# Kernel tuning notes

Hardware: AMD Instinct MI355X
Metric: run time of the kernel (lower is better)

## Reference

```python
import jax, jax.numpy as jnp
import numpy as np

EOS = 1  # EOS_VALUE in the original code (word_label == 1 triggers end_sentence)
L_LAYERS = 2
B, T, H, E = 128, 256, 1024, 1024  # TD == E == input_size


def setup_inputs() -> dict:
    key = jax.random.key(0)
    ks = jax.random.split(key, 20)
    k = 1.0 / np.sqrt(H)
    u = lambda kk, shape: jax.random.uniform(kk, shape, jnp.float32, -k, k)
    inp = {
        "yy_pad": jax.random.randint(ks[0], (B, T), 0, E, dtype=jnp.int32),
        "h_t": jax.random.normal(ks[1], (L_LAYERS, B, H), jnp.float32),
        "h_t_rev": jax.random.normal(ks[2], (L_LAYERS, B, H), jnp.float32),
        "x_lens": jax.random.randint(ks[3], (B,), 1, T - 1, dtype=jnp.int32).at[0].set(T - 1),
        # parameters (layer 0 input size == E == H, so weights stack cleanly)
        "emb": jax.random.normal(ks[4], (E, E), jnp.float32) * 0.02,
        "W_ih": u(ks[5], (L_LAYERS, 4 * H, E)),
        "W_hh": u(ks[6], (L_LAYERS, 4 * H, H)),
        "b_ih": u(ks[7], (L_LAYERS, 4 * H)),
        "b_hh": u(ks[8], (L_LAYERS, 4 * H)),
        "W_ih_rev": u(ks[9], (L_LAYERS, 4 * H, E)),
        "W_hh_rev": u(ks[10], (L_LAYERS, 4 * H, H)),
        "b_ih_rev": u(ks[11], (L_LAYERS, 4 * H)),
        "b_hh_rev": u(ks[12], (L_LAYERS, 4 * H)),
        "c0": jnp.zeros((L_LAYERS, H), jnp.float32),
        "c0_rev": jnp.zeros((L_LAYERS, H), jnp.float32),
        "fc_W": u(ks[13], (E, 2 * H)),
        "fc_b": u(ks[14], (E,)),
    }
    return inp


def _lstm_cell(x, h, c, Wih, Whh, bih, bhh):
    # torch.nn.LSTMCell gate order: input, forget, cell(g), output
    z = x @ Wih.T + bih + h @ Whh.T + bhh  # [B, 4H]
    i, f, g, o = jnp.split(z, 4, axis=-1)
    c2 = jax.nn.sigmoid(f) * c + jax.nn.sigmoid(i) * jnp.tanh(g)
    h2 = jax.nn.sigmoid(o) * jnp.tanh(c2)
    return h2, c2


def reference(yy_pad, h_t, h_t_rev, x_lens, emb, W_ih, W_hh, b_ih, b_hh,
              W_ih_rev, W_hh_rev, b_ih_rev, b_hh_rev, c0, c0_rev, fc_W, fc_b):
    batch = yy_pad.shape[0]
    n_steps = yy_pad.shape[1]  # == max(x_lens) + 1 by construction (static)
    eos_onehot = jax.nn.one_hot(EOS, fc_W.shape[0], dtype=fc_W.dtype)  # [TD]

    c_init = jnp.broadcast_to(c0[:, None, :], (L_LAYERS, batch, c0.shape[1]))
    c_init_rev = jnp.broadcast_to(c0_rev[:, None, :], (L_LAYERS, batch, c0.shape[1]))

    def step(carry, _):
        feed, h, hr, c, cr, ended = carry
        x = emb[feed]   # [B, E]  (sos embedding / previous argmax token)
        xr = x
        hs, hrs, cs, crs = [], [], [], []
        for l in range(L_LAYERS):
            hn, cn = _lstm_cell(x, h[l], c[l], W_ih[l], W_hh[l], b_ih[l], b_hh[l])
            hrn, crn = _lstm_cell(xr, hr[l], cr[l], W_ih_rev[l], W_hh_rev[l], b_ih_rev[l], b_hh_rev[l])
            hs.append(hn); cs.append(cn); hrs.append(hrn); crs.append(crn)
            x, xr = hn, hrn
        h, hr = jnp.stack(hs), jnp.stack(hrs)
        c, cr = jnp.stack(cs), jnp.stack(crs)
        # faithful to torch: cat([B,H],[B,H]) -> [B,2H] -> permute(1,0) -> reshape(B,-1)
        wh = jnp.concatenate([h[-1], hr[-1]], axis=-1).T.reshape(batch, -1)
        logits = wh @ fc_W.T + fc_b  # [B, TD]
        logits = jnp.where(ended[:, None], eos_onehot, logits)
        label = jnp.argmax(logits, axis=1).astype(jnp.int32)
        ended = ended | (label == EOS)
        return (label, h, hr, c, cr, ended), logits

    carry0 = (yy_pad[:, 0], h_t, h_t_rev, c_init, c_init_rev,
              jnp.zeros((batch,), jnp.bool_))
    _, logits_seq = jax.lax.scan(step, carry0, None, length=n_steps)  # [T, B, TD]
    return jax.nn.softmax(jnp.transpose(logits_seq, (1, 0, 2)), axis=-1)  # [B, T, TD]
```

## Files before the change

### kernel.cpp

```cpp
#include <hip/hip_runtime.h>
#include <math.h>

#define NB 128
#define NT 256
#define NH 1024
#define NE 1024
#define G4 4096
#define EOSL 1

#define C_OFF    ((size_t)0)
#define HT_OFF   ((size_t)524288)
#define FCZ_OFF  ((size_t)786432)
#define BIAS_OFF ((size_t)1835008)
#define END_OFF  ((size_t)1851392)
#define XPH_OFF  ((size_t)1851520)
#define XPX_OFF  ((size_t)2900096)
#define WP_OFF   ((size_t)3031168)
#define TOTAL_MIN_F  ((size_t)3031168)
#define TOTAL_PACK_F ((size_t)36585600)

typedef __attribute__((ext_vector_type(8))) short s8v;
typedef __attribute__((ext_vector_type(4))) float f4v;
typedef __attribute__((ext_vector_type(2))) unsigned u2v;

__device__ __forceinline__ float sigmoid_stable(float x) {
  if (x >= 0.f) return 1.f / (1.f + expf(-x));
  float ex = expf(x);
  return ex / (1.f + ex);
}
__device__ __forceinline__ void add4(float4& d, const float4 a) {
  d.x += a.x; d.y += a.y; d.z += a.z; d.w += a.w;
}
__device__ __forceinline__ unsigned short bf_rne(float x) {
  unsigned u = __float_as_uint(x);
  return (unsigned short)((u + 0x7FFFu + ((u >> 16) & 1u)) >> 16);
}
__device__ __forceinline__ void split_bf(float x, unsigned short& h, unsigned short& l) {
  unsigned u = __float_as_uint(x);
  unsigned hb = (u + 0x7FFFu + ((u >> 16) & 1u)) >> 16;
  h = (unsigned short)hb;
  float r = x - __uint_as_float(hb << 16);
  l = bf_rne(r);
}
__device__ __forceinline__ void cvt8(float4 a0, float4 a1, s8v& hi, s8v& lo)
{
  const float v[8] = {a0.x, a0.y, a0.z, a0.w, a1.x, a1.y, a1.z, a1.w};
  #pragma unroll
  for (int j = 0; j < 8; j++) {
    unsigned short h, l; split_bf(v[j], h, l);
    hi[j] = (short)h; lo[j] = (short)l;
  }
}


__global__ void k_init(const int* yy, const float* h_t, const float* h_tr,
                       const float* c0, const float* c0r,
                       const float* b_ih, const float* b_hh,
                       const float* b_ihr, const float* b_hhr,
                       const float* emb,
                       unsigned short* xph, unsigned short* xpx,
                       float* call, float* bias, int* ended)
{
  int idx = blockIdx.x * 256 + threadIdx.x;
  if (idx < 2 * 2048 * 128) {
    int dir = idx / (2048 * 128); int rem = idx % (2048 * 128);
    int row = rem >> 7, b = rem & 127;
    int l = row >> 10, n = row & 1023;
    const float* src = dir ? h_tr : h_t;
    float v = src[((size_t)l * 128 + b) * 1024 + n];
    unsigned short h, lo; split_bf(v, h, lo);
    size_t off = ((size_t)(dir * 64 + (row >> 5)) * 8 + (b >> 4)) * 1024
               + ((b & 15) + 16 * ((n >> 3) & 3)) * 8 + (n & 7);
    xph[off] = h; xph[off + 512] = lo;
  }
  if (idx < 4 * 1024 * 128) {
    int ld = idx / (1024 * 128); int l = ld >> 1;
    int rem = idx % (1024 * 128);
    int mb = rem >> 10, nl = rem & 7;
    const float* cs = (ld & 1) ? c0r : c0;
    call[idx] = cs[l * 1024 + mb * 8 + nl];
  }
  if (idx < 4 * 4096) {
    int ld = idx / 4096; int l = ld >> 1, dir = ld & 1;
    int m = idx & 4095;
    bias[idx] = (dir ? b_ihr : b_ih)[l * 4096 + m] + (dir ? b_hhr : b_hh)[l * 4096 + m];
  }
  if (idx < 128 * 1024) {
    int b = idx >> 10, k = idx & 1023;
    int e = yy[b * NT];
    float v = emb[(size_t)e * 1024 + k];
    unsigned short h, lo; split_bf(v, h, lo);
    size_t off = ((size_t)(k >> 5) * 8 + (b >> 4)) * 1024
               + ((b & 15) + 16 * ((k >> 3) & 3)) * 8 + (k & 7);
    xpx[off] = h; xpx[off + 512] = lo;
  }
  if (idx < NB) ended[idx] = 0;
}

__global__ void k_packW(const float* W_ih, const float* W_hh,
                        const float* W_ihr, const float* W_hhr,
                        unsigned short* WP)
{
  int idx = blockIdx.x * 256 + threadIdx.x;
  int l = idx & 63;
  int frag = idx >> 6;
  int ktile = frag & 63;
  int mtile = (frag >> 6) & 255;
  int ld = frag >> 14;
  int layer = ld >> 1, dir = ld & 1;
  int s = l & 15;
  int mbb = mtile >> 1, half = mtile & 1;
  int gate = half * 2 + (s >> 3);
  int m = gate * 1024 + mbb * 8 + (s & 7);
  int kg = ktile * 32 + (l >> 4) * 8;
  const float* base;
  if (kg < 1024) base = (dir ? W_ihr : W_ih) + ((size_t)layer * 4096 + m) * 1024 + kg;
  else           base = (dir ? W_hhr : W_hh) + ((size_t)layer * 4096 + m) * 1024 + (kg - 1024);
  float4 a0 = *(const float4*)base, a1 = *(const float4*)(base + 4);
  s8v hi, lo; cvt8(a0, a1, hi, lo);
  unsigned short* outp = WP + (size_t)frag * 1024 + l * 8;
  *(s8v*)outp = hi;
  *(s8v*)(outp + 512) = lo;
}

__device__ __forceinline__ void red_write(float* red, int slot, int l, const f4v (&acc)[2][8])
{
  #pragma unroll
  for (int mt = 0; mt < 2; mt++)
    #pragma unroll
    for (int bt = 0; bt < 8; bt++)
      *(f4v*)&red[(size_t)slot * 4096 + (mt * 8 + bt) * 256 + l * 4] = acc[mt][bt];
}
__device__ __forceinline__ void red_add(const float* red, int slot, int l, f4v (&acc)[2][8])
{
  #pragma unroll
  for (int mt = 0; mt < 2; mt++)
    #pragma unroll
    for (int bt = 0; bt < 8; bt++)
      acc[mt][bt] += *(const f4v*)&red[(size_t)slot * 4096 + (mt * 8 + bt) * 256 + l * 4];
}
__device__ __forceinline__ void gloadW(const unsigned short* Wb, int kk,
                                       s8v (&h)[2], s8v (&lo)[2])
{
  #pragma unroll
  for (int mt = 0; mt < 2; mt++) {
    const unsigned short* q = Wb + ((size_t)(mt * 64 + kk) << 10);
    h[mt] = *(const s8v*)q; lo[mt] = *(const s8v*)(q + 512);
  }
}
__device__ __forceinline__ void gloadB(const unsigned short* Bb, int kk,
                                       s8v (&h)[8], s8v (&lo)[8])
{
  #pragma unroll
  for (int bt = 0; bt < 8; bt++) {
    const unsigned short* q = Bb + ((size_t)(kk * 8 + bt) << 10);
    h[bt] = *(const s8v*)q; lo[bt] = *(const s8v*)(q + 512);
  }
}

template<int PACKED>
__device__ __forceinline__ void gemm_k256(f4v (&acc)[2][8],
                                          const unsigned short* Wb,
                                          const float* Wrow0, const float* Wrow1,
                                          const unsigned short* Bb)
{
  if (PACKED) {
    s8v whc[2], wlc[2];
    gloadW(Wb, 0, whc, wlc);
    #pragma unroll 1
    for (int kk = 0; kk < 8; kk++) {
      s8v bh[8], bl[8];
      gloadB(Bb, kk, bh, bl);
      s8v whn[2], wln[2];
      if (kk < 7) gloadW(Wb, kk + 1, whn, wln);
      #pragma unroll
      for (int mt = 0; mt < 2; mt++)
        #pragma unroll
        for (int bt = 0; bt < 8; bt++) {
          acc[mt][bt] = __builtin_amdgcn_mfma_f32_16x16x32_bf16(whc[mt], bh[bt], acc[mt][bt], 0, 0, 0);
          acc[mt][bt] = __builtin_amdgcn_mfma_f32_16x16x32_bf16(whc[mt], bl[bt], acc[mt][bt], 0, 0, 0);
          acc[mt][bt] = __builtin_amdgcn_mfma_f32_16x16x32_bf16(wlc[mt], bh[bt], acc[mt][bt], 0, 0, 0);
        }
      if (kk < 7) {
        whc[0] = whn[0]; whc[1] = whn[1];
        wlc[0] = wln[0]; wlc[1] = wln[1];
      }
    }
  } else {
    const float* Wrow[2] = { Wrow0, Wrow1 };
    float4 ac[2][2];
    #pragma unroll
    for (int mt = 0; mt < 2; mt++) {
      ac[mt][0] = *(const float4*)(Wrow[mt]);
      ac[mt][1] = *(const float4*)(Wrow[mt] + 4);
    }
    #pragma unroll 1
    for (int kk = 0; kk < 8; kk++) {
      s8v bh[8], bl[8];
      gloadB(Bb, kk, bh, bl);
      float4 an[2][2];
      if (kk < 7) {
        #pragma unroll
        for (int mt = 0; mt < 2; mt++) {
          an[mt][0] = *(const float4*)(Wrow[mt] + (kk + 1) * 32);
          an[mt][1] = *(const float4*)(Wrow[mt] + (kk + 1) * 32 + 4);
        }
      }
      #pragma unroll
      for (int mt = 0; mt < 2; mt++) {
        s8v wh, wl;
        cvt8(ac[mt][0], ac[mt][1], wh, wl);
        #pragma unroll
        for (int bt = 0; bt < 8; bt++) {
          acc[mt][bt] = __builtin_amdgcn_mfma_f32_16x16x32_bf16(wh, bh[bt], acc[mt][bt], 0, 0, 0);
          acc[mt][bt] = __builtin_amdgcn_mfma_f32_16x16x32_bf16(wh, bl[bt], acc[mt][bt], 0, 0, 0);
          acc[mt][bt] = __builtin_amdgcn_mfma_f32_16x16x32_bf16(wl, bh[bt], acc[mt][bt], 0, 0, 0);
        }
      }
      if (kk < 7) {
        #pragma unroll
        for (int mt = 0; mt < 2; mt++) { ac[mt][0] = an[mt][0]; ac[mt][1] = an[mt][1]; }
      }
    }
  }
}

__device__ __forceinline__ void reduce_to_zs(float* lds, int tid, int l, int w,
                                             f4v (&acc)[2][8])
{
  if (w >= 4) red_write(lds, w - 4, l, acc);
  __syncthreads();
  if (w < 4) red_add(lds, w, l, acc);
  __syncthreads();
  if (w == 2 || w == 3) red_write(lds, w - 2, l, acc);
  __syncthreads();
  if (w < 2) red_add(lds, w, l, acc);
  __syncthreads();
  if (w < 2) red_write(lds, w, l, acc);
  __syncthreads();
  float* zs = lds + 8192;
  #pragma unroll
  for (int vi = 0; vi < 2; vi++) {
    int v = tid + vi * 512;
    f4v s = *(const f4v*)&lds[(size_t)v * 4];
    s += *(const f4v*)&lds[4096 + (size_t)v * 4];
    int frag = v >> 6, lane = v & 63;
    int mt = frag >> 3, bt = frag & 7;
    int s0 = (lane >> 4) * 4, bcol = bt * 16 + (lane & 15);
    #pragma unroll
    for (int r = 0; r < 4; r++)
      zs[mt * 2048 + (s0 + r) * 128 + bcol] = s[r];
  }
  __syncthreads();
}

struct CellP {
  const unsigned short* WP;
  const float* Wih; const float* Whh; const float* Wihr; const float* Whhr;
  const float* bias; float* c; const unsigned short* xpx; float* Ht;
};

template<int LAYER, int PACKED>
__global__ __launch_bounds__(512, 2) void k_cell(CellP p, const unsigned short* xpR,
                                                 unsigned short* xpW)
{
  __shared__ __align__(16) float lds[16384];
  const int mb = blockIdx.x, dir = blockIdx.y, tid = threadIdx.x;
  const int l = tid & 63, w = tid >> 6;
  const int lr = l & 15, lk = l >> 4;

  const unsigned short* Bb;
  if (LAYER == 0)
    Bb = (w < 4) ? p.xpx + (size_t)w * 65536
                 : xpR + (size_t)(dir * 64 + (w - 4) * 8) * 8192;
  else
    Bb = (w < 4) ? xpW + (size_t)(dir * 64 + w * 8) * 8192
                 : xpR + (size_t)(dir * 64 + 32 + (w - 4) * 8) * 8192;
  Bb += l * 8;

  f4v acc[2][8];
  #pragma unroll
  for (int mt = 0; mt < 2; mt++)
    #pragma unroll
    for (int bt = 0; bt < 8; bt++)
      acc[mt][bt] = (f4v)(0.0f);

  if (PACKED) {
    const unsigned short* Wb = p.WP + (size_t)(LAYER * 2 + dir) * 16777216ULL
        + (((size_t)(mb * 2) * 64 + (size_t)w * 8) << 10) + l * 8;
    gemm_k256<1>(acc, Wb, nullptr, nullptr, Bb);
  } else {
    const float* Wsel = ((w < 4) ? (dir ? p.Wihr : p.Wih) : (dir ? p.Whhr : p.Whh))
                      + (size_t)LAYER * 4194304;
    int col0 = (w & 3) * 256 + lk * 8;
    const float* Wr0 = Wsel + ((size_t)(((lr >> 3)) * 1024 + mb * 8 + (lr & 7))) * 1024 + col0;
    const float* Wr1 = Wsel + ((size_t)((2 + (lr >> 3)) * 1024 + mb * 8 + (lr & 7))) * 1024 + col0;
    gemm_k256<0>(acc, nullptr, Wr0, Wr1, Bb);
  }

  reduce_to_zs(lds, tid, l, w, acc);
  float* zs = lds + 8192;

  int ldg = LAYER * 2 + dir;
  if (tid < 256) {
    int b = tid & 127, q = tid >> 7;
    float* cp = p.c + ((((size_t)ldg * 128 + mb) * 128 + b) * 8 + q * 4);
    f4v cold = *(const f4v*)cp;
    f4v cnew;
    float hs[4];
    #pragma unroll
    for (int j = 0; j < 4; j++) {
      int nl = q * 4 + j;
      int n = mb * 8 + nl;
      float iv = zs[nl * 128 + b]              + p.bias[ldg * 4096 + n];
      float fv = zs[(nl + 8) * 128 + b]        + p.bias[ldg * 4096 + 1024 + n];
      float gv = zs[2048 + nl * 128 + b]       + p.bias[ldg * 4096 + 2048 + n];
      float ov = zs[2048 + (nl + 8) * 128 + b] + p.bias[ldg * 4096 + 3072 + n];
      float co = cold[j];
      float cn = sigmoid_stable(fv) * co + sigmoid_stable(iv) * tanhf(gv);
      float hn = sigmoid_stable(ov) * tanhf(cn);
      cnew[j] = cn;
      hs[j] = hn;
    }
    *(f4v*)cp = cnew;
    unsigned short hh[4], ll[4];
    #pragma unroll
    for (int j = 0; j < 4; j++) split_bf(hs[j], hh[j], ll[j]);
    int kt = LAYER * 32 + (mb >> 2);
    size_t off = ((size_t)(dir * 64 + kt) * 8 + (b >> 4)) * 1024
               + ((size_t)((b & 15) + 16 * (mb & 3))) * 8 + q * 4;
    u2v vh; vh.x = (unsigned)hh[0] | ((unsigned)hh[1] << 16);
            vh.y = (unsigned)hh[2] | ((unsigned)hh[3] << 16);
    u2v vl; vl.x = (unsigned)ll[0] | ((unsigned)ll[1] << 16);
            vl.y = (unsigned)ll[2] | ((unsigned)ll[3] << 16);
    *(u2v*)(xpW + off) = vh;
    *(u2v*)(xpW + off + 512) = vl;
    if (LAYER == 1) {
      #pragma unroll
      for (int j = 0; j < 4; j++) {
        int n = mb * 8 + q * 4 + j;
        p.Ht[(size_t)dir * 131072 + (size_t)n * 128 + b] = hs[j];
      }
    }
  }
}

__global__ __launch_bounds__(256) void k_fc(const float* Ht, const float* fc_W, float* fcz)
{
  int et = blockIdx.x, kp = blockIdx.y;
  int e0 = et * 64;
  int k00 = kp * 256;
  __shared__ __align__(16) float in_s[128][36];
  __shared__ __align__(16) float w_s[64][36];
  int t = threadIdx.x, e_sub = t & 7, bg = t >> 3, b0 = bg * 4;
  float acc[8][4] = {};
  for (int kc = 0; kc < 256; kc += 32) {
    #pragma unroll
    for (int i = 0; i < 4; i++) {
      int flat = t + 256 * i, r = flat >> 3, f4i = flat & 7;
      const float* row = Ht + (r >= 64 ? (size_t)NH * NB + (size_t)(r - 64) * 2048
                                       : (size_t)r * 2048);
      float4 v = *(const float4*)(row + k00 + kc + f4i * 4);
      int sw = (f4i ^ (r >> 2)) & 7;
      *(float4*)&in_s[r][sw * 4] = v;
    }
    #pragma unroll
    for (int i = 0; i < 2; i++) {
      int flat = t + 256 * i, r = flat >> 3, f4i = flat & 7;
      *(float4*)&w_s[r][f4i * 4] =
          *(const float4*)(fc_W + (size_t)(e0 + r) * 2048 + k00 + kc + f4i * 4);
    }
    __syncthreads();
    #pragma unroll
    for (int kq = 0; kq < 8; kq++) {
      int ksw = (kq ^ bg) & 7;
      float4 a4[4];
      #pragma unroll
      for (int ib = 0; ib < 4; ib++) a4[ib] = *(const float4*)&in_s[b0 + ib][ksw * 4];
      float4 w4[8];
      #pragma unroll
      for (int je = 0; je < 8; je++) w4[je] = *(const float4*)&w_s[e_sub + 8 * je][kq * 4];
      #pragma unroll
      for (int je = 0; je < 8; je++)
        #pragma unroll
        for (int ib = 0; ib < 4; ib++)
          acc[je][ib] += a4[ib].x * w4[je].x + a4[ib].y * w4[je].y +
                         a4[ib].z * w4[je].z + a4[ib].w * w4[je].w;
    }
    __syncthreads();
  }
  for (int je = 0; je < 8; je++) {
    int e = e0 + e_sub + 8 * je;
    for (int ib = 0; ib < 4; ib++)
      fcz[((size_t)kp * NB + b0 + ib) * NE + e] = acc[je][ib];
  }
}

__global__ void k_final(const float* fcz, const float* fc_b, int* ended,
                        float* out, int tstep, const float* emb, unsigned short* xpx)
{
  int b = blockIdx.x;
  int t = threadIdx.x;
  __shared__ float sval[256];
  __shared__ int   sidx[256];
  __shared__ float ssum[256];
  bool end = (ended[b] != 0);
  float v[4];
  int e_base = t * 4;
  float4 vv = *(const float4*)&fc_b[e_base];
  #pragma unroll
  for (int p = 0; p < 8; p++)
    add4(vv, *(const float4*)&fcz[((size_t)p * NB + b) * NE + e_base]);
  v[0] = vv.x; v[1] = vv.y; v[2] = vv.z; v[3] = vv.w;
  if (end) {
    #pragma unroll
    for (int j = 0; j < 4; j++) v[j] = (e_base + j == EOSL) ? 1.f : 0.f;
  }
  float bv = v[0]; int bi = e_base;
  #pragma unroll
  for (int j = 1; j < 4; j++) if (v[j] > bv) { bv = v[j]; bi = e_base + j; }
  sval[t] = bv; sidx[t] = bi;
  __syncthreads();
  for (int s = 128; s > 0; s >>= 1) {
    if (t < s) {
      float ov = sval[t + s]; int oi = sidx[t + s];
      if (ov > sval[t] || (ov == sval[t] && oi < sidx[t])) { sval[t] = ov; sidx[t] = oi; }
    }
    __syncthreads();
  }
  float m = sval[0]; int label = sidx[0];
  {
    int k0 = t * 4;
    float4 e4 = *(const float4*)(emb + (size_t)label * 1024 + k0);
    size_t off = ((size_t)(k0 >> 5) * 8 + (b >> 4)) * 1024
               + ((b & 15) + 16 * ((k0 >> 3) & 3)) * 8 + (k0 & 7);
    ushort4 h4, l4;
    unsigned short hh, ll;
    split_bf(e4.x, hh, ll); h4.x = hh; l4.x = ll;
    split_bf(e4.y, hh, ll); h4.y = hh; l4.y = ll;
    split_bf(e4.z, hh, ll); h4.z = hh; l4.z = ll;
    split_bf(e4.w, hh, ll); h4.w = hh; l4.w = ll;
    *(ushort4*)(xpx + off) = h4;
    *(ushort4*)(xpx + off + 512) = l4;
  }
  float ls = 0.f;
  #pragma unroll
  for (int j = 0; j < 4; j++) { v[j] = expf(v[j] - m); ls += v[j]; }
  ssum[t] = ls;
  __syncthreads();
  for (int s = 128; s > 0; s >>= 1) { if (t < s) ssum[t] += ssum[t + s]; __syncthreads(); }
  float inv = 1.f / ssum[0];
  float* orow = out + ((size_t)b * NT + tstep) * NE + e_base;
  #pragma unroll
  for (int j = 0; j < 4; j++) orow[j] = v[j] * inv;
  if (t == 0) ended[b] = (end || label == EOSL) ? 1 : 0;
}

extern "C" void kernel_launch(void* const* d_in, const int* in_sizes, int n_in,
                              void* d_out, int out_size, void* d_ws, size_t ws_size,
                              hipStream_t stream)
{
  const int*   yy    = (const int*)d_in[0];
  const float* h_t   = (const float*)d_in[1];
  const float* h_tr  = (const float*)d_in[2];
  const float* emb   = (const float*)d_in[4];
  const float* W_ih  = (const float*)d_in[5];
  const float* W_hh  = (const float*)d_in[6];
  const float* b_ih  = (const float*)d_in[7];
  const float* b_hh  = (const float*)d_in[8];
  const float* W_ihr = (const float*)d_in[9];
  const float* W_hhr = (const float*)d_in[10];
  const float* b_ihr = (const float*)d_in[11];
  const float* b_hhr = (const float*)d_in[12];
  const float* c0    = (const float*)d_in[13];
  const float* c0r   = (const float*)d_in[14];
  const float* fc_W  = (const float*)d_in[15];
  const float* fc_b  = (const float*)d_in[16];
  float* out = (float*)d_out;

  float* ws = (float*)d_ws;
  float* call = ws + C_OFF;
  float* Ht   = ws + HT_OFF;
  float* fcz  = ws + FCZ_OFF;
  float* bias = ws + BIAS_OFF;
  int* ended  = (int*)(ws + END_OFF);
  unsigned short* xph = (unsigned short*)(ws + XPH_OFF);
  unsigned short* xpx = (unsigned short*)(ws + XPX_OFF);
  unsigned short* WP  = (unsigned short*)(ws + WP_OFF);
  bool packed = ws_size >= TOTAL_PACK_F * sizeof(float);

  k_init<<<2048, 256, 0, stream>>>(yy, h_t, h_tr, c0, c0r, b_ih, b_hh, b_ihr, b_hhr,
                                   emb, xph, xpx, call, bias, ended);
  if (packed)
    k_packW<<<16384, 256, 0, stream>>>(W_ih, W_hh, W_ihr, W_hhr, WP);

  CellP cp;
  cp.WP = WP;
  cp.Wih = W_ih; cp.Whh = W_hh; cp.Wihr = W_ihr; cp.Whhr = W_hhr;
  cp.bias = bias; cp.c = call; cp.xpx = xpx; cp.Ht = Ht;

  for (int t = 0; t < NT; t++) {
    const unsigned short* xpR = xph + (size_t)(t & 1) * 1048576;
    unsigned short* xpW = xph + (size_t)((t & 1) ^ 1) * 1048576;
    if (packed) {
      k_cell<0, 1><<<dim3(128, 2), 512, 0, stream>>>(cp, xpR, xpW);
      k_cell<1, 1><<<dim3(128, 2), 512, 0, stream>>>(cp, xpR, xpW);
    } else {
      k_cell<0, 0><<<dim3(128, 2), 512, 0, stream>>>(cp, xpR, xpW);
      k_cell<1, 0><<<dim3(128, 2), 512, 0, stream>>>(cp, xpR, xpW);
    }
    k_fc<<<dim3(16, 8), 256, 0, stream>>>(Ht, fc_W, fcz);
    k_final<<<128, 256, 0, stream>>>(fcz, fc_b, ended, out, t, emb, xpx);
  }
}
```

Before: 22.78 ms.

## Halve per-block hidden tile in LSTM cell and double FC split-K

Each cell block now computes 4 hidden units (16 gate rows as one MFMA tile) instead of 8, so the grid doubles to 256x2 blocks. Weight packing, c-state layout and the epilogue are reorganised to match. LDS drops and launch bounds rise to allow more resident blocks. The FC projection is also split into 16 K-chunks instead of 8 for more blocks. The aim is to fill more compute units on this latency-bound recurrent step, at the cost of more partial-sum traffic and narrower scalar stores.

```diff
diff --git a/kernel.cpp b/kernel.cpp
--- a/kernel.cpp
+++ b/kernel.cpp
@@ -11,17 +11,16 @@
 #define C_OFF    ((size_t)0)
 #define HT_OFF   ((size_t)524288)
 #define FCZ_OFF  ((size_t)786432)
-#define BIAS_OFF ((size_t)1835008)
-#define END_OFF  ((size_t)1851392)
-#define XPH_OFF  ((size_t)1851520)
-#define XPX_OFF  ((size_t)2900096)
-#define WP_OFF   ((size_t)3031168)
-#define TOTAL_MIN_F  ((size_t)3031168)
-#define TOTAL_PACK_F ((size_t)36585600)
+#define BIAS_OFF ((size_t)2883584)
+#define END_OFF  ((size_t)2899968)
+#define XPH_OFF  ((size_t)2900096)
+#define XPX_OFF  ((size_t)3948672)
+#define WP_OFF   ((size_t)4079744)
+#define TOTAL_MIN_F  ((size_t)4079744)
+#define TOTAL_PACK_F ((size_t)37634176)
 
 typedef __attribute__((ext_vector_type(8))) short s8v;
 typedef __attribute__((ext_vector_type(4))) float f4v;
-typedef __attribute__((ext_vector_type(2))) unsigned u2v;
 
 __device__ __forceinline__ float sigmoid_stable(float x) {
   if (x >= 0.f) return 1.f / (1.f + expf(-x));
@@ -76,9 +75,9 @@
   if (idx < 4 * 1024 * 128) {
     int ld = idx / (1024 * 128); int l = ld >> 1;
     int rem = idx % (1024 * 128);
-    int mb = rem >> 10, nl = rem & 7;
+    int n = rem >> 7;
     const float* cs = (ld & 1) ? c0r : c0;
-    call[idx] = cs[l * 1024 + mb * 8 + nl];
+    call[idx] = cs[l * 1024 + n];
   }
   if (idx < 4 * 4096) {
     int ld = idx / 4096; int l = ld >> 1, dir = ld & 1;
@@ -105,13 +104,12 @@
   int l = idx & 63;
   int frag = idx >> 6;
   int ktile = frag & 63;
-  int mtile = (frag >> 6) & 255;
+  int mq = (frag >> 6) & 255;
   int ld = frag >> 14;
   int layer = ld >> 1, dir = ld & 1;
   int s = l & 15;
-  int mbb = mtile >> 1, half = mtile & 1;
-  int gate = half * 2 + (s >> 3);
-  int m = gate * 1024 + mbb * 8 + (s & 7);
+  int gate = s >> 2;
+  int m = gate * 1024 + mq * 4 + (s & 3);
   int kg = ktile * 32 + (l >> 4) * 8;
   const float* base;
   if (kg < 1024) base = (dir ? W_ihr : W_ih) + ((size_t)layer * 4096 + m) * 1024 + kg;
@@ -123,30 +121,17 @@
   *(s8v*)(outp + 512) = lo;
 }
 
-__device__ __forceinline__ void red_write(float* red, int slot, int l, const f4v (&acc)[2][8])
-{
-  #pragma unroll
-  for (int mt = 0; mt < 2; mt++)
-    #pragma unroll
-    for (int bt = 0; bt < 8; bt++)
-      *(f4v*)&red[(size_t)slot * 4096 + (mt * 8 + bt) * 256 + l * 4] = acc[mt][bt];
-}
-__device__ __forceinline__ void red_add(const float* red, int slot, int l, f4v (&acc)[2][8])
-{
-  #pragma unroll
-  for (int mt = 0; mt < 2; mt++)
-    #pragma unroll
-    for (int bt = 0; bt < 8; bt++)
-      acc[mt][bt] += *(const f4v*)&red[(size_t)slot * 4096 + (mt * 8 + bt) * 256 + l * 4];
-}
-__device__ __forceinline__ void gloadW(const unsigned short* Wb, int kk,
-                                       s8v (&h)[2], s8v (&lo)[2])
-{
-  #pragma unroll
-  for (int mt = 0; mt < 2; mt++) {
-    const unsigned short* q = Wb + ((size_t)(mt * 64 + kk) << 10);
-    h[mt] = *(const s8v*)q; lo[mt] = *(const s8v*)(q + 512);
-  }
+__device__ __forceinline__ void red_write8(float* red, int slot, int l, const f4v (&acc)[8])
+{
+  #pragma unroll
+  for (int bt = 0; bt < 8; bt++)
+    *(f4v*)&red[(size_t)slot * 2048 + bt * 256 + l * 4] = acc[bt];
+}
+__device__ __forceinline__ void red_add8(const float* red, int slot, int l, f4v (&acc)[8])
+{
+  #pragma unroll
+  for (int bt = 0; bt < 8; bt++)
+    acc[bt] += *(const f4v*)&red[(size_t)slot * 2048 + bt * 256 + l * 4];
 }
 __device__ __forceinline__ void gloadB(const unsigned short* Bb, int kk,
                                        s8v (&h)[8], s8v (&lo)[8])
@@ -156,102 +141,6 @@
     const unsigned short* q = Bb + ((size_t)(kk * 8 + bt) << 10);
     h[bt] = *(const s8v*)q; lo[bt] = *(const s8v*)(q + 512);
   }
-}
-
-template<int PACKED>
-__device__ __forceinline__ void gemm_k256(f4v (&acc)[2][8],
-                                          const unsigned short* Wb,
-                                          const float* Wrow0, const float* Wrow1,
-                                          const unsigned short* Bb)
-{
-  if (PACKED) {
-    s8v whc[2], wlc[2];
-    gloadW(Wb, 0, whc, wlc);
-    #pragma unroll 1
-    for (int kk = 0; kk < 8; kk++) {
-      s8v bh[8], bl[8];
-      gloadB(Bb, kk, bh, bl);
-      s8v whn[2], wln[2];
-      if (kk < 7) gloadW(Wb, kk + 1, whn, wln);
-      #pragma unroll
-      for (int mt = 0; mt < 2; mt++)
-        #pragma unroll
-        for (int bt = 0; bt < 8; bt++) {
-          acc[mt][bt] = __builtin_amdgcn_mfma_f32_16x16x32_bf16(whc[mt], bh[bt], acc[mt][bt], 0, 0, 0);
-          acc[mt][bt] = __builtin_amdgcn_mfma_f32_16x16x32_bf16(whc[mt], bl[bt], acc[mt][bt], 0, 0, 0);
-          acc[mt][bt] = __builtin_amdgcn_mfma_f32_16x16x32_bf16(wlc[mt], bh[bt], acc[mt][bt], 0, 0, 0);
-        }
-      if (kk < 7) {
-        whc[0] = whn[0]; whc[1] = whn[1];
-        wlc[0] = wln[0]; wlc[1] = wln[1];
-      }
-    }
-  } else {
-    const float* Wrow[2] = { Wrow0, Wrow1 };
-    float4 ac[2][2];
-    #pragma unroll
-    for (int mt = 0; mt < 2; mt++) {
-      ac[mt][0] = *(const float4*)(Wrow[mt]);
-      ac[mt][1] = *(const float4*)(Wrow[mt] + 4);
-    }
-    #pragma unroll 1
-    for (int kk = 0; kk < 8; kk++) {
-      s8v bh[8], bl[8];
-      gloadB(Bb, kk, bh, bl);
-      float4 an[2][2];
-      if (kk < 7) {
-        #pragma unroll
-        for (int mt = 0; mt < 2; mt++) {
-          an[mt][0] = *(const float4*)(Wrow[mt] + (kk + 1) * 32);
-          an[mt][1] = *(const float4*)(Wrow[mt] + (kk + 1) * 32 + 4);
-        }
-      }
-      #pragma unroll
-      for (int mt = 0; mt < 2; mt++) {
-        s8v wh, wl;
-        cvt8(ac[mt][0], ac[mt][1], wh, wl);
-        #pragma unroll
-        for (int bt = 0; bt < 8; bt++) {
-          acc[mt][bt] = __builtin_amdgcn_mfma_f32_16x16x32_bf16(wh, bh[bt], acc[mt][bt], 0, 0, 0);
-          acc[mt][bt] = __builtin_amdgcn_mfma_f32_16x16x32_bf16(wh, bl[bt], acc[mt][bt], 0, 0, 0);
-          acc[mt][bt] = __builtin_amdgcn_mfma_f32_16x16x32_bf16(wl, bh[bt], acc[mt][bt], 0, 0, 0);
-        }
-      }
-      if (kk < 7) {
-        #pragma unroll
-        for (int mt = 0; mt < 2; mt++) { ac[mt][0] = an[mt][0]; ac[mt][1] = an[mt][1]; }
-      }
-    }
-  }
-}
-
-__device__ __forceinline__ void reduce_to_zs(float* lds, int tid, int l, int w,
-                                             f4v (&acc)[2][8])
-{
-  if (w >= 4) red_write(lds, w - 4, l, acc);
-  __syncthreads();
-  if (w < 4) red_add(lds, w, l, acc);
-  __syncthreads();
-  if (w == 2 || w == 3) red_write(lds, w - 2, l, acc);
-  __syncthreads();
-  if (w < 2) red_add(lds, w, l, acc);
-  __syncthreads();
-  if (w < 2) red_write(lds, w, l, acc);
-  __syncthreads();
-  float* zs = lds + 8192;
-  #pragma unroll
-  for (int vi = 0; vi < 2; vi++) {
-    int v = tid + vi * 512;
-    f4v s = *(const f4v*)&lds[(size_t)v * 4];
-    s += *(const f4v*)&lds[4096 + (size_t)v * 4];
-    int frag = v >> 6, lane = v & 63;
-    int mt = frag >> 3, bt = frag & 7;
-    int s0 = (lane >> 4) * 4, bcol = bt * 16 + (lane & 15);
-    #pragma unroll
-    for (int r = 0; r < 4; r++)
-      zs[mt * 2048 + (s0 + r) * 128 + bcol] = s[r];
-  }
-  __syncthreads();
 }
 
 struct CellP {
@@ -261,11 +150,11 @@
 };
 
 template<int LAYER, int PACKED>
-__global__ __launch_bounds__(512, 2) void k_cell(CellP p, const unsigned short* xpR,
+__global__ __launch_bounds__(512, 4) void k_cell(CellP p, const unsigned short* xpR,
                                                  unsigned short* xpW)
 {
-  __shared__ __align__(16) float lds[16384];
-  const int mb = blockIdx.x, dir = blockIdx.y, tid = threadIdx.x;
+  __shared__ __align__(16) float lds[10240];
+  const int mq = blockIdx.x, dir = blockIdx.y, tid = threadIdx.x;
   const int l = tid & 63, w = tid >> 6;
   const int lr = l & 15, lk = l >> 4;
 
@@ -278,70 +167,101 @@
                  : xpR + (size_t)(dir * 64 + 32 + (w - 4) * 8) * 8192;
   Bb += l * 8;
 
-  f4v acc[2][8];
-  #pragma unroll
-  for (int mt = 0; mt < 2; mt++)
-    #pragma unroll
-    for (int bt = 0; bt < 8; bt++)
-      acc[mt][bt] = (f4v)(0.0f);
+  f4v acc[8];
+  #pragma unroll
+  for (int bt = 0; bt < 8; bt++) acc[bt] = (f4v)(0.0f);
 
   if (PACKED) {
     const unsigned short* Wb = p.WP + (size_t)(LAYER * 2 + dir) * 16777216ULL
-        + (((size_t)(mb * 2) * 64 + (size_t)w * 8) << 10) + l * 8;
-    gemm_k256<1>(acc, Wb, nullptr, nullptr, Bb);
+        + (((size_t)mq * 64 + (size_t)w * 8) << 10) + l * 8;
+    s8v whc = *(const s8v*)Wb, wlc = *(const s8v*)(Wb + 512);
+    #pragma unroll 1
+    for (int kk = 0; kk < 8; kk++) {
+      s8v bh[8], bl[8];
+      gloadB(Bb, kk, bh, bl);
+      s8v whn, wln;
+      if (kk < 7) {
+        const unsigned short* q = Wb + ((size_t)(kk + 1) << 10);
+        whn = *(const s8v*)q; wln = *(const s8v*)(q + 512);
+      }
+      #pragma unroll
+      for (int bt = 0; bt < 8; bt++) {
+        acc[bt] = __builtin_amdgcn_mfma_f32_16x16x32_bf16(whc, bh[bt], acc[bt], 0, 0, 0);
+        acc[bt] = __builtin_amdgcn_mfma_f32_16x16x32_bf16(whc, bl[bt], acc[bt], 0, 0, 0);
+        acc[bt] = __builtin_amdgcn_mfma_f32_16x16x32_bf16(wlc, bh[bt], acc[bt], 0, 0, 0);
+      }
+      if (kk < 7) { whc = whn; wlc = wln; }
+    }
   } else {
     const float* Wsel = ((w < 4) ? (dir ? p.Wihr : p.Wih) : (dir ? p.Whhr : p.Whh))
                       + (size_t)LAYER * 4194304;
     int col0 = (w & 3) * 256 + lk * 8;
-    const float* Wr0 = Wsel + ((size_t)(((lr >> 3)) * 1024 + mb * 8 + (lr & 7))) * 1024 + col0;
-    const float* Wr1 = Wsel + ((size_t)((2 + (lr >> 3)) * 1024 + mb * 8 + (lr & 7))) * 1024 + col0;
-    gemm_k256<0>(acc, nullptr, Wr0, Wr1, Bb);
-  }
-
-  reduce_to_zs(lds, tid, l, w, acc);
+    int m = (lr >> 2) * 1024 + mq * 4 + (lr & 3);
+    const float* Wr = Wsel + (size_t)m * 1024 + col0;
+    float4 ac0 = *(const float4*)Wr, ac1 = *(const float4*)(Wr + 4);
+    #pragma unroll 1
+    for (int kk = 0; kk < 8; kk++) {
+      s8v bh[8], bl[8];
+      gloadB(Bb, kk, bh, bl);
+      float4 an0, an1;
+      if (kk < 7) {
+        an0 = *(const float4*)(Wr + (kk + 1) * 32);
+        an1 = *(const float4*)(Wr + (kk + 1) * 32 + 4);
+      }
+      s8v wh, wl;
+      cvt8(ac0, ac1, wh, wl);
+      #pragma unroll
+      for (int bt = 0; bt < 8; bt++) {
+        acc[bt] = __builtin_amdgcn_mfma_f32_16x16x32_bf16(wh, bh[bt], acc[bt], 0, 0, 0);
+        acc[bt] = __builtin_amdgcn_mfma_f32_16x16x32_bf16(wh, bl[bt], acc[bt], 0, 0, 0);
+        acc[bt] = __builtin_amdgcn_mfma_f32_16x16x32_bf16(wl, bh[bt], acc[bt], 0, 0, 0);
+      }
+      if (kk < 7) { ac0 = an0; ac1 = an1; }
+    }
+  }
+
+  if (w >= 4) red_write8(lds, w - 4, l, acc);
+  __syncthreads();
+  if (w < 4) red_add8(lds, w, l, acc);
+  __syncthreads();
+  if (w == 2 || w == 3) red_write8(lds, w - 2, l, acc);
+  __syncthreads();
+  if (w < 2) red_add8(lds, w, l, acc);
+  __syncthreads();
+  if (w < 2) red_write8(lds, w, l, acc);
+  __syncthreads();
   float* zs = lds + 8192;
-
-  int ldg = LAYER * 2 + dir;
-  if (tid < 256) {
-    int b = tid & 127, q = tid >> 7;
-    float* cp = p.c + ((((size_t)ldg * 128 + mb) * 128 + b) * 8 + q * 4);
-    f4v cold = *(const f4v*)cp;
-    f4v cnew;
-    float hs[4];
+  {
+    f4v s = *(const f4v*)&lds[(size_t)tid * 4];
+    s += *(const f4v*)&lds[2048 + (size_t)tid * 4];
+    int bt = tid >> 6, ll = tid & 63;
     #pragma unroll
-    for (int j = 0; j < 4; j++) {
-      int nl = q * 4 + j;
-      int n = mb * 8 + nl;
-      float iv = zs[nl * 128 + b]              + p.bias[ldg * 4096 + n];
-      float fv = zs[(nl + 8) * 128 + b]        + p.bias[ldg * 4096 + 1024 + n];
-      float gv = zs[2048 + nl * 128 + b]       + p.bias[ldg * 4096 + 2048 + n];
-      float ov = zs[2048 + (nl + 8) * 128 + b] + p.bias[ldg * 4096 + 3072 + n];
-      float co = cold[j];
-      float cn = sigmoid_stable(fv) * co + sigmoid_stable(iv) * tanhf(gv);
-      float hn = sigmoid_stable(ov) * tanhf(cn);
-      cnew[j] = cn;
-      hs[j] = hn;
-    }
-    *(f4v*)cp = cnew;
-    unsigned short hh[4], ll[4];
-    #pragma unroll
-    for (int j = 0; j < 4; j++) split_bf(hs[j], hh[j], ll[j]);
-    int kt = LAYER * 32 + (mb >> 2);
+    for (int r = 0; r < 4; r++)
+      zs[((ll >> 4) * 4 + r) * 128 + bt * 16 + (ll & 15)] = s[r];
+  }
+  __syncthreads();
+
+  {
+    int ldg = LAYER * 2 + dir;
+    int b = tid & 127, nl = tid >> 7;
+    int n = mq * 4 + nl;
+    float iv = zs[nl * 128 + b]        + p.bias[ldg * 4096 + n];
+    float fv = zs[(4 + nl) * 128 + b]  + p.bias[ldg * 4096 + 1024 + n];
+    float gv = zs[(8 + nl) * 128 + b]  + p.bias[ldg * 4096 + 2048 + n];
+    float ov = zs[(12 + nl) * 128 + b] + p.bias[ldg * 4096 + 3072 + n];
+    float* cp = p.c + ((size_t)ldg * 1024 + n) * 128 + b;
+    float cold = *cp;
+    float cn = sigmoid_stable(fv) * cold + sigmoid_stable(iv) * tanhf(gv);
+    float hn = sigmoid_stable(ov) * tanhf(cn);
+    *cp = cn;
+    unsigned short hh, lo; split_bf(hn, hh, lo);
+    int kt = LAYER * 32 + (n >> 5), n5 = n & 31;
     size_t off = ((size_t)(dir * 64 + kt) * 8 + (b >> 4)) * 1024
-               + ((size_t)((b & 15) + 16 * (mb & 3))) * 8 + q * 4;
-    u2v vh; vh.x = (unsigned)hh[0] | ((unsigned)hh[1] << 16);
-            vh.y = (unsigned)hh[2] | ((unsigned)hh[3] << 16);
-    u2v vl; vl.x = (unsigned)ll[0] | ((unsigned)ll[1] << 16);
-            vl.y = (unsigned)ll[2] | ((unsigned)ll[3] << 16);
-    *(u2v*)(xpW + off) = vh;
-    *(u2v*)(xpW + off + 512) = vl;
-    if (LAYER == 1) {
-      #pragma unroll
-      for (int j = 0; j < 4; j++) {
-        int n = mb * 8 + q * 4 + j;
-        p.Ht[(size_t)dir * 131072 + (size_t)n * 128 + b] = hs[j];
-      }
-    }
+               + ((size_t)((b & 15) + 16 * ((n5 >> 3) & 3))) * 8 + (n5 & 7);
+    xpW[off] = hh;
+    xpW[off + 512] = lo;
+    if (LAYER == 1)
+      p.Ht[(size_t)dir * 131072 + (size_t)n * 128 + b] = hn;
   }
 }
 
@@ -349,18 +269,16 @@
 {
   int et = blockIdx.x, kp = blockIdx.y;
   int e0 = et * 64;
-  int k00 = kp * 256;
+  int k00 = kp * 128;
   __shared__ __align__(16) float in_s[128][36];
   __shared__ __align__(16) float w_s[64][36];
   int t = threadIdx.x, e_sub = t & 7, bg = t >> 3, b0 = bg * 4;
   float acc[8][4] = {};
-  for (int kc = 0; kc < 256; kc += 32) {
+  for (int kc = 0; kc < 128; kc += 32) {
     #pragma unroll
     for (int i = 0; i < 4; i++) {
       int flat = t + 256 * i, r = flat >> 3, f4i = flat & 7;
-      const float* row = Ht + (r >= 64 ? (size_t)NH * NB + (size_t)(r - 64) * 2048
-                                       : (size_t)r * 2048);
-      float4 v = *(const float4*)(row + k00 + kc + f4i * 4);
+      float4 v = *(const float4*)(Ht + (size_t)r * 2048 + k00 + kc + f4i * 4);
       int sw = (f4i ^ (r >> 2)) & 7;
       *(float4*)&in_s[r][sw * 4] = v;
     }
@@ -409,7 +327,7 @@
   int e_base = t * 4;
   float4 vv = *(const float4*)&fc_b[e_base];
   #pragma unroll
-  for (int p = 0; p < 8; p++)
+  for (int p = 0; p < 16; p++)
     add4(vv, *(const float4*)&fcz[((size_t)p * NB + b) * NE + e_base]);
   v[0] = vv.x; v[1] = vv.y; v[2] = vv.z; v[3] = vv.w;
   if (end) {
@@ -503,13 +421,13 @@
     const unsigned short* xpR = xph + (size_t)(t & 1) * 1048576;
     unsigned short* xpW = xph + (size_t)((t & 1) ^ 1) * 1048576;
     if (packed) {
-      k_cell<0, 1><<<dim3(128, 2), 512, 0, stream>>>(cp, xpR, xpW);
-      k_cell<1, 1><<<dim3(128, 2), 512, 0, stream>>>(cp, xpR, xpW);
+      k_cell<0, 1><<<dim3(256, 2), 512, 0, stream>>>(cp, xpR, xpW);
+      k_cell<1, 1><<<dim3(256, 2), 512, 0, stream>>>(cp, xpR, xpW);
     } else {
-      k_cell<0, 0><<<dim3(128, 2), 512, 0, stream>>>(cp, xpR, xpW);
-      k_cell<1, 0><<<dim3(128, 2), 512, 0, stream>>>(cp, xpR, xpW);
-    }
-    k_fc<<<dim3(16, 8), 256, 0, stream>>>(Ht, fc_W, fcz);
+      k_cell<0, 0><<<dim3(256, 2), 512, 0, stream>>>(cp, xpR, xpW);
+      k_cell<1, 0><<<dim3(256, 2), 512, 0, stream>>>(cp, xpR, xpW);
+    }
+    k_fc<<<dim3(16, 16), 256, 0, stream>>>(Ht, fc_W, fcz);
     k_final<<<128, 256, 0, stream>>>(fcz, fc_b, ended, out, t, emb, xpx);
   }
 }
```

Result: faster. 21.25 ms (-6.7%).
